# Kernel optimization log

Measured on AMD Instinct MI355X. Metric: run time of the kernel, lower is better.

## Reference

```python
import jax, jax.numpy as jnp
import numpy as np

EPS = 1e-05
EPS_SQRT = EPS ** 0.5


def setup_inputs() -> dict:
    key = jax.random.key(0)
    x = jax.random.normal(key, (4, 2048, 4096), dtype=jnp.float32)
    weight = jnp.ones((4096,), dtype=jnp.float32)
    bias = jnp.zeros((4096,), dtype=jnp.float32)
    return {"x": x, "weight": weight, "bias": bias}


def _sign_nz(v):
    # sign() with 0 mapped to +1 (matches torch code: x_sign[x_sign==0]=1)
    s = jnp.sign(v)
    return jnp.where(s == 0, 1.0, s)


def _layer_normal_norm(x, weight, bias):
    # standardize over last dim (biased variance, correction=0)
    mean = jnp.mean(x, axis=-1, keepdims=True)
    var = jnp.var(x, axis=-1, keepdims=True)
    xs = (x - mean) / jnp.sqrt(var + EPS)

    x_sign = _sign_nz(xs)
    x_abs = jnp.abs(xs)
    l1p = jnp.log1p(x_abs)

    # Newton estimate of lambda (order 2)
    s1 = jnp.mean(x_sign * l1p, axis=-1, keepdims=True)
    d = (1.0 + x_abs) * l1p - x_abs
    dvar = 2.0 * jnp.mean(xs * d, axis=-1, keepdims=True)
    g1 = 0.5 * dvar - s1

    dmean = jnp.mean(d, axis=-1, keepdims=True)
    d_sub_sq = jnp.square(d - dmean)
    p1 = (1.0 + x_abs) * jnp.square(l1p) - 2.0 * d
    d2 = x_sign * p1
    d2var = 2.0 * jnp.mean(xs * d2 + d_sub_sq, axis=-1, keepdims=True)
    g2 = -0.5 * jnp.square(dvar) + 0.5 * d2var

    lmbda = 1.0 - g1 / (g2 + EPS_SQRT)  # broadcasts to full [B,S,D]

    # power transform
    eta = 1.0 + x_sign * (lmbda - 1.0)
    eta_sign = jax.lax.stop_gradient(_sign_nz(eta))
    exponent = eta + eta_sign * EPS_SQRT
    x_tr1 = (x_sign / exponent) * (jnp.power(1.0 + x_abs, exponent) - 1.0)
    x_tr2 = x_sign * l1p
    mask = jax.lax.stop_gradient(jnp.abs(eta) <= EPS_SQRT)
    x_tr = jnp.where(mask, x_tr2, x_tr1)

    # eval mode: no additive noise (self.training == False)
    return x_tr * weight + bias


def reference(x, weight, bias):
    return _layer_normal_norm(x, weight, bias)
```

## Files before the change

kernel.cpp:

```cpp
#include <hip/hip_runtime.h>
#include <math.h>

#define D 4096
#define NT 256
#define PER 16
#define EPS 1e-5f
#define EPS_SQRT 3.16227766016837933e-3f
#define LN2 0.69314718055994531f
#define NBLOCKS 2048

__global__ __launch_bounds__(NT) void lnn_kernel(const float* __restrict__ x,
                                                 const float* __restrict__ w,
                                                 const float* __restrict__ b,
                                                 float* __restrict__ out,
                                                 int rows, int rpb) {
    const int tid = threadIdx.x;
    const int wave = tid >> 6;
    const int r0 = blockIdx.x * rpb;
    int r1 = r0 + rpb; if (r1 > rows) r1 = rows;
    if (r0 >= r1) return;

    __shared__ float red1[4][2];
    __shared__ float red2[4][5];

    const float inv_d = 1.f / (float)D;

    float v[PER];
    {
        const float4* x4 = (const float4*)(x + (size_t)r0 * D);
#pragma unroll
        for (int c = 0; c < 4; ++c) {
            float4 f = x4[c * NT + tid];
            v[c*4+0] = f.x; v[c*4+1] = f.y; v[c*4+2] = f.z; v[c*4+3] = f.w;
        }
    }

    for (int r = r0; r < r1; ++r) {
        const bool pn = (r + 1 < r1);
        float n[PER];
        if (pn) {
            const float4* nx4 = (const float4*)(x + (size_t)(r + 1) * D);
#pragma unroll
            for (int c = 0; c < 4; ++c) {
                float4 f = nx4[c * NT + tid];
                n[c*4+0] = f.x; n[c*4+1] = f.y; n[c*4+2] = f.z; n[c*4+3] = f.w;
            }
        }

        float s = 0.f, s2 = 0.f;
#pragma unroll
        for (int i = 0; i < PER; ++i) { s += v[i]; s2 = fmaf(v[i], v[i], s2); }
#pragma unroll
        for (int o = 32; o > 0; o >>= 1) {
            s  += __shfl_down(s,  o, 64);
            s2 += __shfl_down(s2, o, 64);
        }
        if ((tid & 63) == 0) { red1[wave][0] = s; red1[wave][1] = s2; }
        __syncthreads();
        s  = red1[0][0] + red1[1][0] + red1[2][0] + red1[3][0];
        s2 = red1[0][1] + red1[1][1] + red1[2][1] + red1[3][1];
        const float mean = s * inv_d;
        const float var  = s2 * inv_d - mean * mean;
        const float rstd = rsqrtf(var + EPS);
        const float nm   = -mean * rstd;

        float s1 = 0.f, sxd = 0.f, sd = 0.f, sd2 = 0.f, sxd2 = 0.f;
#pragma unroll
        for (int i = 0; i < PER; ++i) {
            float xs   = fmaf(v[i], rstd, nm);
            float ab   = fabsf(xs);
            float onea = 1.f + ab;
            float L2   = __builtin_amdgcn_logf(onea);
            float sv   = copysignf(L2, xs);
            v[i] = sv;
            s1 += sv;
            float l  = L2 * LN2;
            float dd = fmaf(onea, l, -ab);
            sxd = fmaf(xs, dd, sxd);
            sd += dd;
            sd2 = fmaf(dd, dd, sd2);
            float p1 = fmaf(onea, l * l, -(dd + dd));
            sxd2 = fmaf(ab, p1, sxd2);
        }

        float4 wfs[4], bfs[4];
        {
            const float4* w4 = (const float4*)w;
            const float4* b4 = (const float4*)b;
#pragma unroll
            for (int c = 0; c < 4; ++c) {
                wfs[c] = w4[c * NT + tid];
                bfs[c] = b4[c * NT + tid];
            }
        }

#pragma unroll
        for (int o = 32; o > 0; o >>= 1) {
            s1   += __shfl_down(s1,   o, 64);
            sxd  += __shfl_down(sxd,  o, 64);
            sd   += __shfl_down(sd,   o, 64);
            sd2  += __shfl_down(sd2,  o, 64);
            sxd2 += __shfl_down(sxd2, o, 64);
        }
        if ((tid & 63) == 0) {
            red2[wave][0] = s1; red2[wave][1] = sxd; red2[wave][2] = sd;
            red2[wave][3] = sd2; red2[wave][4] = sxd2;
        }
        __syncthreads();
        s1   = red2[0][0] + red2[1][0] + red2[2][0] + red2[3][0];
        sxd  = red2[0][1] + red2[1][1] + red2[2][1] + red2[3][1];
        sd   = red2[0][2] + red2[1][2] + red2[2][2] + red2[3][2];
        sd2  = red2[0][3] + red2[1][3] + red2[2][3] + red2[3][3];
        sxd2 = red2[0][4] + red2[1][4] + red2[2][4] + red2[3][4];

        const float s1m   = s1 * (inv_d * LN2);
        const float dvar  = 2.f * sxd * inv_d;
        const float g1    = 0.5f * dvar - s1m;
        const float dmean = sd * inv_d;
        const float vard  = sd2 * inv_d - dmean * dmean;
        const float d2var = 2.f * (sxd2 * inv_d + vard);
        const float g2    = -0.5f * dvar * dvar + 0.5f * d2var;
        const float lm    = 1.f - g1 * __builtin_amdgcn_rcpf(g2 + EPS_SQRT);

        const float eta_p = lm;
        const float eta_n = 2.f - lm;
        const float ep = eta_p + ((eta_p >= 0.f) ? EPS_SQRT : -EPS_SQRT);
        const float en = eta_n + ((eta_n >= 0.f) ? EPS_SQRT : -EPS_SQRT);
        const bool  mp = fabsf(eta_p) <= EPS_SQRT;
        const bool  mn = fabsf(eta_n) <= EPS_SQRT;
        const float rp =  __builtin_amdgcn_rcpf(ep);
        const float rn = -__builtin_amdgcn_rcpf(en);

        float* orow = out + (size_t)r * D;

        if (!(mp || mn)) {
#pragma unroll
            for (int c = 0; c < 4; ++c) {
                float wa[4] = {wfs[c].x, wfs[c].y, wfs[c].z, wfs[c].w};
                float ba[4] = {bfs[c].x, bfs[c].y, bfs[c].z, bfs[c].w};
                float oa[4];
#pragma unroll
                for (int j = 0; j < 4; ++j) {
                    float sv = v[c*4 + j];
                    bool pos = (sv >= 0.f);
                    float L2 = fabsf(sv);
                    float e  = pos ? ep : en;
                    float re = pos ? rp : rn;
                    float tr = fmaf(re, __builtin_amdgcn_exp2f(e * L2), -re);
                    oa[j] = fmaf(tr, wa[j], ba[j]);
                }
                float4 o = {oa[0], oa[1], oa[2], oa[3]};
                ((float4*)orow)[c * NT + tid] = o;
            }
        } else {
#pragma unroll
            for (int c = 0; c < 4; ++c) {
                float wa[4] = {wfs[c].x, wfs[c].y, wfs[c].z, wfs[c].w};
                float ba[4] = {bfs[c].x, bfs[c].y, bfs[c].z, bfs[c].w};
                float oa[4];
#pragma unroll
                for (int j = 0; j < 4; ++j) {
                    float sv = v[c*4 + j];
                    bool pos = (sv >= 0.f);
                    float L2 = fabsf(sv);
                    float e  = pos ? ep : en;
                    float re = pos ? rp : rn;
                    bool  m  = pos ? mp : mn;
                    float tr1 = fmaf(re, __builtin_amdgcn_exp2f(e * L2), -re);
                    float tr2 = sv * LN2;
                    float tr  = m ? tr2 : tr1;
                    oa[j] = fmaf(tr, wa[j], ba[j]);
                }
                float4 o = {oa[0], oa[1], oa[2], oa[3]};
                ((float4*)orow)[c * NT + tid] = o;
            }
        }

        if (pn) {
#pragma unroll
            for (int i = 0; i < PER; ++i) v[i] = n[i];
        }
    }
}

extern "C" void kernel_launch(void* const* d_in, const int* in_sizes, int n_in,
                              void* d_out, int out_size, void* d_ws, size_t ws_size,
                              hipStream_t stream) {
    const float* x = (const float*)d_in[0];
    const float* w = (const float*)d_in[1];
    const float* b = (const float*)d_in[2];
    float* out = (float*)d_out;
    const int rows = in_sizes[0] / D;
    int nblocks = NBLOCKS;
    if (nblocks > rows) nblocks = rows;
    const int rpb = (rows + nblocks - 1) / nblocks;
    lnn_kernel<<<dim3(nblocks), dim3(NT), 0, stream>>>(x, w, b, out, rows, rpb);
}
```

Measured before the change: 238.8 us.

## Map one row per wavefront and drop block-level shared-memory reductions

Each 64-lane wavefront now processes a whole 4096-element row, holding 64 values per lane in registers, and reduces with xor shuffles only. This removes the two __syncthreads and LDS exchanges per row, along with the persistent multi-row loop and its next-row prefetch. The launch becomes one block of 4 waves per 4 rows. Register pressure rises sharply (64-float arrays), which can lower occupancy, and the software prefetch that overlapped loads with compute is gone.

New measurement: 274.1 us. +14.8%, slower.

```diff
diff --git a/kernel.cpp b/kernel.cpp
--- a/kernel.cpp
+++ b/kernel.cpp
@@ -2,183 +2,139 @@
 #include <math.h>
 
 #define D 4096
-#define NT 256
-#define PER 16
+#define NW 4
+#define NT (64 * NW)
 #define EPS 1e-5f
 #define EPS_SQRT 3.16227766016837933e-3f
 #define LN2 0.69314718055994531f
-#define NBLOCKS 2048
 
-__global__ __launch_bounds__(NT) void lnn_kernel(const float* __restrict__ x,
-                                                 const float* __restrict__ w,
-                                                 const float* __restrict__ b,
-                                                 float* __restrict__ out,
-                                                 int rows, int rpb) {
-    const int tid = threadIdx.x;
-    const int wave = tid >> 6;
-    const int r0 = blockIdx.x * rpb;
-    int r1 = r0 + rpb; if (r1 > rows) r1 = rows;
-    if (r0 >= r1) return;
+__global__ __launch_bounds__(NT, 4) void lnn_kernel(const float* __restrict__ x,
+                                                    const float* __restrict__ w,
+                                                    const float* __restrict__ b,
+                                                    float* __restrict__ out,
+                                                    int rows) {
+    const int lane = threadIdx.x & 63;
+    const int wv   = threadIdx.x >> 6;
+    const int row  = blockIdx.x * NW + wv;
+    if (row >= rows) return;
 
-    __shared__ float red1[4][2];
-    __shared__ float red2[4][5];
+    const float4* x4 = (const float4*)(x + (size_t)row * D);
+
+    float v[64];
+#pragma unroll
+    for (int c = 0; c < 16; ++c) {
+        float4 f = x4[c * 64 + lane];
+        v[c*4+0] = f.x; v[c*4+1] = f.y; v[c*4+2] = f.z; v[c*4+3] = f.w;
+    }
 
     const float inv_d = 1.f / (float)D;
 
-    float v[PER];
-    {
-        const float4* x4 = (const float4*)(x + (size_t)r0 * D);
+    float s = 0.f, s2 = 0.f;
 #pragma unroll
-        for (int c = 0; c < 4; ++c) {
-            float4 f = x4[c * NT + tid];
-            v[c*4+0] = f.x; v[c*4+1] = f.y; v[c*4+2] = f.z; v[c*4+3] = f.w;
-        }
+    for (int i = 0; i < 64; ++i) { s += v[i]; s2 = fmaf(v[i], v[i], s2); }
+#pragma unroll
+    for (int m = 32; m > 0; m >>= 1) {
+        s  += __shfl_xor(s,  m, 64);
+        s2 += __shfl_xor(s2, m, 64);
+    }
+    const float mean = s * inv_d;
+    const float var  = s2 * inv_d - mean * mean;
+    const float rstd = rsqrtf(var + EPS);
+    const float nm   = -mean * rstd;
+
+    float s1 = 0.f, sxd = 0.f, sd = 0.f, sd2 = 0.f, sxd2 = 0.f;
+#pragma unroll
+    for (int i = 0; i < 64; ++i) {
+        float xs   = fmaf(v[i], rstd, nm);
+        float ab   = fabsf(xs);
+        float onea = 1.f + ab;
+        float L2   = __builtin_amdgcn_logf(onea);
+        float sv   = copysignf(L2, xs);
+        v[i] = sv;
+        s1 += sv;
+        float l  = L2 * LN2;
+        float dd = fmaf(onea, l, -ab);
+        sxd = fmaf(xs, dd, sxd);
+        sd += dd;
+        sd2 = fmaf(dd, dd, sd2);
+        float p1 = fmaf(onea, l * l, -(dd + dd));
+        sxd2 = fmaf(ab, p1, sxd2);
+    }
+#pragma unroll
+    for (int m = 32; m > 0; m >>= 1) {
+        s1   += __shfl_xor(s1,   m, 64);
+        sxd  += __shfl_xor(sxd,  m, 64);
+        sd   += __shfl_xor(sd,   m, 64);
+        sd2  += __shfl_xor(sd2,  m, 64);
+        sxd2 += __shfl_xor(sxd2, m, 64);
     }
 
-    for (int r = r0; r < r1; ++r) {
-        const bool pn = (r + 1 < r1);
-        float n[PER];
-        if (pn) {
-            const float4* nx4 = (const float4*)(x + (size_t)(r + 1) * D);
+    const float s1m   = s1 * (inv_d * LN2);
+    const float dvar  = 2.f * sxd * inv_d;
+    const float g1    = 0.5f * dvar - s1m;
+    const float dmean = sd * inv_d;
+    const float vard  = sd2 * inv_d - dmean * dmean;
+    const float d2var = 2.f * (sxd2 * inv_d + vard);
+    const float g2    = -0.5f * dvar * dvar + 0.5f * d2var;
+    const float lm    = 1.f - g1 * __builtin_amdgcn_rcpf(g2 + EPS_SQRT);
+
+    const float eta_p = lm;
+    const float eta_n = 2.f - lm;
+    const float ep = eta_p + ((eta_p >= 0.f) ? EPS_SQRT : -EPS_SQRT);
+    const float en = eta_n + ((eta_n >= 0.f) ? EPS_SQRT : -EPS_SQRT);
+    const bool  mp = fabsf(eta_p) <= EPS_SQRT;
+    const bool  mn = fabsf(eta_n) <= EPS_SQRT;
+    const float rp =  __builtin_amdgcn_rcpf(ep);
+    const float rn = -__builtin_amdgcn_rcpf(en);
+
+    float* orow = out + (size_t)row * D;
+    const float4* w4 = (const float4*)w;
+    const float4* b4 = (const float4*)b;
+
+    if (!(mp || mn)) {
 #pragma unroll
-            for (int c = 0; c < 4; ++c) {
-                float4 f = nx4[c * NT + tid];
-                n[c*4+0] = f.x; n[c*4+1] = f.y; n[c*4+2] = f.z; n[c*4+3] = f.w;
+        for (int c = 0; c < 16; ++c) {
+            float4 wf = w4[c * 64 + lane];
+            float4 bf = b4[c * 64 + lane];
+            float wa[4] = {wf.x, wf.y, wf.z, wf.w};
+            float ba[4] = {bf.x, bf.y, bf.z, bf.w};
+            float oa[4];
+#pragma unroll
+            for (int j = 0; j < 4; ++j) {
+                float sv = v[c*4 + j];
+                bool pos = (sv >= 0.f);
+                float L2 = fabsf(sv);
+                float e  = pos ? ep : en;
+                float re = pos ? rp : rn;
+                float tr = fmaf(re, __builtin_amdgcn_exp2f(e * L2), -re);
+                oa[j] = fmaf(tr, wa[j], ba[j]);
             }
+            float4 o = {oa[0], oa[1], oa[2], oa[3]};
+            ((float4*)orow)[c * 64 + lane] = o;
         }
-
-        float s = 0.f, s2 = 0.f;
+    } else {
 #pragma unroll
-        for (int i = 0; i < PER; ++i) { s += v[i]; s2 = fmaf(v[i], v[i], s2); }
+        for (int c = 0; c < 16; ++c) {
+            float4 wf = w4[c * 64 + lane];
+            float4 bf = b4[c * 64 + lane];
+            float wa[4] = {wf.x, wf.y, wf.z, wf.w};
+            float ba[4] = {bf.x, bf.y, bf.z, bf.w};
+            float oa[4];
 #pragma unroll
-        for (int o = 32; o > 0; o >>= 1) {
-            s  += __shfl_down(s,  o, 64);
-            s2 += __shfl_down(s2, o, 64);
-        }
-        if ((tid & 63) == 0) { red1[wave][0] = s; red1[wave][1] = s2; }
-        __syncthreads();
-        s  = red1[0][0] + red1[1][0] + red1[2][0] + red1[3][0];
-        s2 = red1[0][1] + red1[1][1] + red1[2][1] + red1[3][1];
-        const float mean = s * inv_d;
-        const float var  = s2 * inv_d - mean * mean;
-        const float rstd = rsqrtf(var + EPS);
-        const float nm   = -mean * rstd;
-
-        float s1 = 0.f, sxd = 0.f, sd = 0.f, sd2 = 0.f, sxd2 = 0.f;
-#pragma unroll
-        for (int i = 0; i < PER; ++i) {
-            float xs   = fmaf(v[i], rstd, nm);
-            float ab   = fabsf(xs);
-            float onea = 1.f + ab;
-            float L2   = __builtin_amdgcn_logf(onea);
-            float sv   = copysignf(L2, xs);
-            v[i] = sv;
-            s1 += sv;
-            float l  = L2 * LN2;
-            float dd = fmaf(onea, l, -ab);
-            sxd = fmaf(xs, dd, sxd);
-            sd += dd;
-            sd2 = fmaf(dd, dd, sd2);
-            float p1 = fmaf(onea, l * l, -(dd + dd));
-            sxd2 = fmaf(ab, p1, sxd2);
-        }
-
-        float4 wfs[4], bfs[4];
-        {
-            const float4* w4 = (const float4*)w;
-            const float4* b4 = (const float4*)b;
-#pragma unroll
-            for (int c = 0; c < 4; ++c) {
-                wfs[c] = w4[c * NT + tid];
-                bfs[c] = b4[c * NT + tid];
+            for (int j = 0; j < 4; ++j) {
+                float sv = v[c*4 + j];
+                bool pos = (sv >= 0.f);
+                float L2 = fabsf(sv);
+                float e  = pos ? ep : en;
+                float re = pos ? rp : rn;
+                bool  m  = pos ? mp : mn;
+                float tr1 = fmaf(re, __builtin_amdgcn_exp2f(e * L2), -re);
+                float tr2 = sv * LN2;
+                float tr  = m ? tr2 : tr1;
+                oa[j] = fmaf(tr, wa[j], ba[j]);
             }
-        }
-
-#pragma unroll
-        for (int o = 32; o > 0; o >>= 1) {
-            s1   += __shfl_down(s1,   o, 64);
-            sxd  += __shfl_down(sxd,  o, 64);
-            sd   += __shfl_down(sd,   o, 64);
-            sd2  += __shfl_down(sd2,  o, 64);
-            sxd2 += __shfl_down(sxd2, o, 64);
-        }
-        if ((tid & 63) == 0) {
-            red2[wave][0] = s1; red2[wave][1] = sxd; red2[wave][2] = sd;
-            red2[wave][3] = sd2; red2[wave][4] = sxd2;
-        }
-        __syncthreads();
-        s1   = red2[0][0] + red2[1][0] + red2[2][0] + red2[3][0];
-        sxd  = red2[0][1] + red2[1][1] + red2[2][1] + red2[3][1];
-        sd   = red2[0][2] + red2[1][2] + red2[2][2] + red2[3][2];
-        sd2  = red2[0][3] + red2[1][3] + red2[2][3] + red2[3][3];
-        sxd2 = red2[0][4] + red2[1][4] + red2[2][4] + red2[3][4];
-
-        const float s1m   = s1 * (inv_d * LN2);
-        const float dvar  = 2.f * sxd * inv_d;
-        const float g1    = 0.5f * dvar - s1m;
-        const float dmean = sd * inv_d;
-        const float vard  = sd2 * inv_d - dmean * dmean;
-        const float d2var = 2.f * (sxd2 * inv_d + vard);
-        const float g2    = -0.5f * dvar * dvar + 0.5f * d2var;
-        const float lm    = 1.f - g1 * __builtin_amdgcn_rcpf(g2 + EPS_SQRT);
-
-        const float eta_p = lm;
-        const float eta_n = 2.f - lm;
-        const float ep = eta_p + ((eta_p >= 0.f) ? EPS_SQRT : -EPS_SQRT);
-        const float en = eta_n + ((eta_n >= 0.f) ? EPS_SQRT : -EPS_SQRT);
-        const bool  mp = fabsf(eta_p) <= EPS_SQRT;
-        const bool  mn = fabsf(eta_n) <= EPS_SQRT;
-        const float rp =  __builtin_amdgcn_rcpf(ep);
-        const float rn = -__builtin_amdgcn_rcpf(en);
-
-        float* orow = out + (size_t)r * D;
-
-        if (!(mp || mn)) {
-#pragma unroll
-            for (int c = 0; c < 4; ++c) {
-                float wa[4] = {wfs[c].x, wfs[c].y, wfs[c].z, wfs[c].w};
-                float ba[4] = {bfs[c].x, bfs[c].y, bfs[c].z, bfs[c].w};
-                float oa[4];
-#pragma unroll
-                for (int j = 0; j < 4; ++j) {
-                    float sv = v[c*4 + j];
-                    bool pos = (sv >= 0.f);
-                    float L2 = fabsf(sv);
-                    float e  = pos ? ep : en;
-                    float re = pos ? rp : rn;
-                    float tr = fmaf(re, __builtin_amdgcn_exp2f(e * L2), -re);
-                    oa[j] = fmaf(tr, wa[j], ba[j]);
-                }
-                float4 o = {oa[0], oa[1], oa[2], oa[3]};
-                ((float4*)orow)[c * NT + tid] = o;
-            }
-        } else {
-#pragma unroll
-            for (int c = 0; c < 4; ++c) {
-                float wa[4] = {wfs[c].x, wfs[c].y, wfs[c].z, wfs[c].w};
-                float ba[4] = {bfs[c].x, bfs[c].y, bfs[c].z, bfs[c].w};
-                float oa[4];
-#pragma unroll
-                for (int j = 0; j < 4; ++j) {
-                    float sv = v[c*4 + j];
-                    bool pos = (sv >= 0.f);
-                    float L2 = fabsf(sv);
-                    float e  = pos ? ep : en;
-                    float re = pos ? rp : rn;
-                    bool  m  = pos ? mp : mn;
-                    float tr1 = fmaf(re, __builtin_amdgcn_exp2f(e * L2), -re);
-                    float tr2 = sv * LN2;
-                    float tr  = m ? tr2 : tr1;
-                    oa[j] = fmaf(tr, wa[j], ba[j]);
-                }
-                float4 o = {oa[0], oa[1], oa[2], oa[3]};
-                ((float4*)orow)[c * NT + tid] = o;
-            }
-        }
-
-        if (pn) {
-#pragma unroll
-            for (int i = 0; i < PER; ++i) v[i] = n[i];
+            float4 o = {oa[0], oa[1], oa[2], oa[3]};
+            ((float4*)orow)[c * 64 + lane] = o;
         }
     }
 }
@@ -191,8 +147,6 @@
     const float* b = (const float*)d_in[2];
     float* out = (float*)d_out;
     const int rows = in_sizes[0] / D;
-    int nblocks = NBLOCKS;
-    if (nblocks > rows) nblocks = rows;
-    const int rpb = (rows + nblocks - 1) / nblocks;
-    lnn_kernel<<<dim3(nblocks), dim3(NT), 0, stream>>>(x, w, b, out, rows, rpb);
+    const int nblocks = (rows + NW - 1) / NW;
+    lnn_kernel<<<dim3(nblocks), dim3(NT), 0, stream>>>(x, w, b, out, rows);
 }
```
